# Performance work log

Measured on AMD Instinct MI355X. Metric: run time of the kernel, lower is better.

Reference implementation:

```python
import jax, jax.numpy as jnp
import numpy as np

N_NODES = 100000
N_FEAT = 512
HIDDEN = 16
N_CLASSES = 7
N_EDGES = 3200000


def gcn_conv(x, W, b, src, dst, num_nodes):
    """GCNConv: add self-loops, symmetric deg^-1/2 normalization, linear, aggregate."""
    loop = jnp.arange(num_nodes, dtype=src.dtype)
    src2 = jnp.concatenate([src, loop])  # [E+N]
    dst2 = jnp.concatenate([dst, loop])
    ones = jnp.ones(src2.shape[0], dtype=x.dtype)
    deg = jax.ops.segment_sum(ones, dst2, num_segments=num_nodes)  # in-degree incl. self-loop
    dinv = jnp.where(deg > 0, jax.lax.rsqrt(deg), 0.0)
    norm = dinv[src2] * dinv[dst2]  # [E+N]
    h = x @ W  # [N, out] -- transform before gather (small out dim)
    msg = h[src2] * norm[:, None]  # gather + scale
    out = jax.ops.segment_sum(msg, dst2, num_segments=num_nodes)  # scatter-add
    return out + b


def setup_inputs() -> dict:
    key = jax.random.key(0)
    k1, k2, k3, k4, k5 = jax.random.split(key, 5)
    x = jax.random.normal(k1, (N_NODES, N_FEAT), dtype=jnp.float32)
    edge_index = jax.random.randint(k2, (2, N_EDGES), 0, N_NODES, dtype=jnp.int64)
    # Glorot init like PyG GCNConv
    W1 = jax.random.normal(k3, (N_FEAT, HIDDEN), dtype=jnp.float32) * np.sqrt(2.0 / (N_FEAT + HIDDEN))
    b1 = jnp.zeros((HIDDEN,), dtype=jnp.float32)
    W2 = jax.random.normal(k4, (HIDDEN, N_CLASSES), dtype=jnp.float32) * np.sqrt(2.0 / (HIDDEN + N_CLASSES))
    b2 = jnp.zeros((N_CLASSES,), dtype=jnp.float32)
    return {"x": x, "edge_index": edge_index, "W1": W1, "b1": b1, "W2": W2, "b2": b2}


def reference(x, edge_index, W1, b1, W2, b2):
    src, dst = edge_index[0], edge_index[1]
    h = gcn_conv(x, W1, b1, src, dst, N_NODES)
    h = jax.nn.relu(h)
    # F.dropout(training=self.training): identity in eval mode (deterministic reference)
    h = gcn_conv(h, W2, b2, src, dst, N_NODES)
    return jax.nn.log_softmax(h, axis=1)
```

## Files before the change

kernel.cpp:

```cpp
#include <hip/hip_runtime.h>
#include <math.h>

#define N_NODES   100000
#define N_FEAT    512
#define HIDDEN    16
#define N_CLASSES 7
#define N_EDGES   3200000

#define BSHIFT 7
#define BNODES 128
#define BMASK  127
#define NBUK   782
#define CHUNK  16384
#define NCHUNK 196
#define CAP    6144

typedef short v8s __attribute__((ext_vector_type(8)));
typedef float v4f __attribute__((ext_vector_type(4)));

__device__ __forceinline__ float bf_lo(unsigned int p) { return __uint_as_float(p << 16); }
__device__ __forceinline__ float bf_hi(unsigned int p) { return __uint_as_float(p & 0xffff0000u); }
__device__ __forceinline__ unsigned int pack_bf2(float a, float b) {
    unsigned int ua = __float_as_uint(a); ua += 0x7fffu + ((ua >> 16) & 1u);
    unsigned int ub = __float_as_uint(b); ub += 0x7fffu + ((ub >> 16) & 1u);
    return (ua >> 16) | (ub & 0xffff0000u);
}


__global__ __launch_bounds__(1024) void k_hist(const int* __restrict__ dst,
                                               int* __restrict__ hglob) {
    __shared__ int h[NBUK];
    int tid = threadIdx.x;
    for (int i = tid; i < NBUK; i += 1024) h[i] = 0;
    __syncthreads();
    int base = blockIdx.x * CHUNK;
    for (int i = tid; i < CHUNK; i += 1024) {
        int e = base + i;
        if (e < N_EDGES) atomicAdd(&h[dst[e] >> BSHIFT], 1);
    }
    __syncthreads();
    for (int i = tid; i < NBUK; i += 1024)
        hglob[blockIdx.x * NBUK + i] = h[i];
}


__global__ __launch_bounds__(1024) void k_scan(const int* __restrict__ hglob,
                                               int* __restrict__ btot,
                                               int* __restrict__ gbase,
                                               int* __restrict__ hpre) {
    __shared__ int sd[1024];
    int t = threadIdx.x;
    int tot = 0;
    if (t < NBUK)
        for (int c = 0; c < NCHUNK; c++) tot += hglob[c * NBUK + t];
    sd[t] = (t < NBUK) ? tot : 0;
    __syncthreads();
    for (int off = 1; off < 1024; off <<= 1) {
        int a = (t >= off) ? sd[t - off] : 0;
        __syncthreads();
        sd[t] += a;
        __syncthreads();
    }
    if (t < NBUK) {
        int ex = sd[t] - tot;
        btot[t] = tot;
        gbase[t] = ex;
        int run = ex;
        for (int c = 0; c < NCHUNK; c++) {
            hpre[c * NBUK + t] = run;
            run += hglob[c * NBUK + t];
        }
    }
}


__global__ __launch_bounds__(1024) void k_scatter(const int* __restrict__ src,
                                                  const int* __restrict__ dst,
                                                  const int* __restrict__ hpre,
                                                  int* __restrict__ entries) {
    __shared__ int lb[NBUK];
    __shared__ int cur[NBUK];
    int tid = threadIdx.x;
    for (int i = tid; i < NBUK; i += 1024) {
        lb[i] = hpre[blockIdx.x * NBUK + i];
        cur[i] = 0;
    }
    __syncthreads();
    int base = blockIdx.x * CHUNK;
    for (int i = tid; i < CHUNK; i += 1024) {
        int e = base + i;
        if (e < N_EDGES) {
            int d = dst[e];
            int b = d >> BSHIFT;
            int pos = lb[b] + atomicAdd(&cur[b], 1);
            entries[pos] = src[e] | ((d & BMASK) << 17);
        }
    }
}


__global__ __launch_bounds__(512) void k_nodesort(int* __restrict__ entries,
                                                  const int* __restrict__ btot,
                                                  const int* __restrict__ gbase,
                                                  float* __restrict__ dinv,
                                                  int* __restrict__ nodeptr) {
    __shared__ int ebuf[CAP];
    __shared__ int hcnt[BNODES];
    __shared__ int hincl[BNODES];
    __shared__ int hcur[BNODES];
    int tid = threadIdx.x;
    int bk = blockIdx.x;
    int cnt = btot[bk], base = gbase[bk];
    if (cnt > CAP) cnt = CAP;
    if (tid < BNODES) hcnt[tid] = 0;
    __syncthreads();
    for (int i = tid; i < cnt; i += 512) {
        int en = entries[base + i];
        ebuf[i] = en;
        atomicAdd(&hcnt[en >> 17], 1);
    }
    __syncthreads();
    if (tid < BNODES) hincl[tid] = hcnt[tid];
    __syncthreads();
    for (int off = 1; off < BNODES; off <<= 1) {
        int v = 0;
        if (tid < BNODES && tid >= off) v = hincl[tid - off];
        __syncthreads();
        if (tid < BNODES) hincl[tid] += v;
        __syncthreads();
    }
    if (tid < BNODES) {
        int excl = hincl[tid] - hcnt[tid];
        hcur[tid] = excl;
        int n = bk * BNODES + tid;
        if (n < N_NODES) {
            nodeptr[n] = base + excl;
            dinv[n]    = rsqrtf((float)(hcnt[tid] + 1));
        } else if (n == N_NODES) {
            nodeptr[n] = base + excl;
        }
    }
    __syncthreads();
    for (int i = tid; i < cnt; i += 512) {
        int en = ebuf[i];
        int pos = atomicAdd(&hcur[en >> 17], 1);
        entries[base + pos] = en & 0x1FFFF;
    }
}


__global__ __launch_bounds__(256) void k_gemm1(const float* __restrict__ x,
                                               const float* __restrict__ W1,
                                               const float* __restrict__ dinv,
                                               unsigned int* __restrict__ hs1b) {
    __shared__ unsigned int wfrag[16 * 64 * 4];
    __shared__ unsigned int atile[64 * 68];

    int tid = threadIdx.x;
    int wave = tid >> 6, lane = tid & 63;
    int row0 = blockIdx.x * 64;
    int m = lane & 15, quad = lane >> 4;

    {
        int q0 = tid * 4;
#pragma unroll
        for (int qq = 0; qq < 4; qq++) {
            int q = q0 + qq;
            int s = q >> 6, l = q & 63;
            int n = l & 15, kb = s * 32 + (l >> 4) * 8;
            unsigned int* wp = &wfrag[q * 4];
#pragma unroll
            for (int h = 0; h < 4; h++)
                wp[h] = pack_bf2(W1[(kb + 2 * h) * 16 + n],
                                 W1[(kb + 2 * h + 1) * 16 + n]);
        }
    }

    v4f acc = {0.f, 0.f, 0.f, 0.f};

    for (int c = 0; c < 4; c++) {
        __syncthreads();
#pragma unroll
        for (int i = 0; i < 8; i++) {
            int f = i * 256 + tid;
            int r = f >> 5, c4 = f & 31;
            int grow = row0 + r;
            float4 xv = make_float4(0.f, 0.f, 0.f, 0.f);
            if (grow < N_NODES)
                xv = *(const float4*)(x + (size_t)grow * N_FEAT + c * 128 + c4 * 4);
            unsigned int* ap = &atile[r * 68 + c4 * 2];
            ap[0] = pack_bf2(xv.x, xv.y);
            ap[1] = pack_bf2(xv.z, xv.w);
        }
        __syncthreads();
#pragma unroll
        for (int s = 0; s < 4; s++) {
            v8s af = *(const v8s*)&atile[(wave * 16 + m) * 68 + s * 16 + quad * 4];
            v8s bf = *(const v8s*)&wfrag[((c * 4 + s) * 64 + lane) * 4];
            acc = __builtin_amdgcn_mfma_f32_16x16x32_bf16(af, bf, acc, 0, 0, 0);
        }
    }

    __syncthreads();
    float* dt = (float*)atile;
    {
        float* wdt = dt + wave * 272;
        int col = lane & 15;
#pragma unroll
        for (int r = 0; r < 4; r++)
            wdt[(quad * 4 + r) * 17 + col] = acc[r];
    }
    __syncthreads();
    {
        int row = tid >> 2, p = tid & 3;
        int grow = row0 + row;
        if (grow < N_NODES) {
            float dn = dinv[grow];
            float* wdt = dt + (row >> 4) * 272 + (row & 15) * 17 + 4 * p;
            unsigned int d0 = pack_bf2(dn * wdt[0], dn * wdt[1]);
            unsigned int d1 = pack_bf2(dn * wdt[2], dn * wdt[3]);
            *(uint2*)(hs1b + (size_t)grow * 8 + 2 * p) = make_uint2(d0, d1);
        }
    }
}


__global__ __launch_bounds__(512) void k_agg1(const unsigned int* __restrict__ hs1b,
                                              const int* __restrict__ srt,
                                              const int* __restrict__ nodeptr,
                                              const float* __restrict__ dinv,
                                              const float* __restrict__ b1,
                                              const float* __restrict__ W2,
                                              unsigned int* __restrict__ hs2b) {
    __shared__ float w2l[HIDDEN * N_CLASSES];
    __shared__ float b1l[HIDDEN];
    __shared__ float part[BNODES][17];
    int tid = threadIdx.x;
    if (tid < HIDDEN * N_CLASSES) w2l[tid] = W2[tid];
    if (tid < HIDDEN) b1l[tid] = b1[tid];

    int bk = blockIdx.x;
    int g = tid >> 1, j = tid & 1;
    int l = g & (BNODES - 1), half = g >> 7;
    int n = bk * BNODES + l;
    bool valid = (n < N_NODES);

    float accL[4] = {0.f, 0.f, 0.f, 0.f};
    float accH[4] = {0.f, 0.f, 0.f, 0.f};
    const uint4* hv = (const uint4*)hs1b;

    if (valid) {
        int p0 = nodeptr[n], p1 = nodeptr[n + 1];
        int mid = p0 + ((p1 - p0) >> 1);
        int e0 = half ? mid : p0;
        int e1 = half ? p1 : mid;
        int e = e0;
        for (; e + 4 <= e1; e += 4) {
            int s[4];
            uint4 v[4];
#pragma unroll
            for (int u = 0; u < 4; u++) s[u] = srt[e + u];
#pragma unroll
            for (int u = 0; u < 4; u++) v[u] = hv[(size_t)s[u] * 2 + j];
#pragma unroll
            for (int u = 0; u < 4; u++) {
                accL[0] += bf_lo(v[u].x); accH[0] += bf_hi(v[u].x);
                accL[1] += bf_lo(v[u].y); accH[1] += bf_hi(v[u].y);
                accL[2] += bf_lo(v[u].z); accH[2] += bf_hi(v[u].z);
                accL[3] += bf_lo(v[u].w); accH[3] += bf_hi(v[u].w);
            }
        }
        for (; e < e1; e++) {
            uint4 v0 = hv[(size_t)srt[e] * 2 + j];
            accL[0] += bf_lo(v0.x); accH[0] += bf_hi(v0.x);
            accL[1] += bf_lo(v0.y); accH[1] += bf_hi(v0.y);
            accL[2] += bf_lo(v0.z); accH[2] += bf_hi(v0.z);
            accL[3] += bf_lo(v0.w); accH[3] += bf_hi(v0.w);
        }
        if (half == 0) {
            uint4 sv = hv[(size_t)n * 2 + j];
            accL[0] += bf_lo(sv.x); accH[0] += bf_hi(sv.x);
            accL[1] += bf_lo(sv.y); accH[1] += bf_hi(sv.y);
            accL[2] += bf_lo(sv.z); accH[2] += bf_hi(sv.z);
            accL[3] += bf_lo(sv.w); accH[3] += bf_hi(sv.w);
        }
    }

    if (half == 1 && valid) {
#pragma unroll
        for (int q = 0; q < 4; q++) {
            int ch = j * 8 + 2 * q;
            part[l][ch]     = accL[q];
            part[l][ch + 1] = accH[q];
        }
    }
    __syncthreads();

    if (half == 0 && valid) {
        float dn = dinv[n];
        float t[7] = {0.f, 0.f, 0.f, 0.f, 0.f, 0.f, 0.f};
#pragma unroll
        for (int q = 0; q < 4; q++) {
            int ch = j * 8 + 2 * q;
            float z0 = fmaxf(dn * (accL[q] + part[l][ch])     + b1l[ch],     0.f);
            float z1 = fmaxf(dn * (accH[q] + part[l][ch + 1]) + b1l[ch + 1], 0.f);
            const float* w0 = &w2l[ch * 7];
            const float* w1 = &w2l[(ch + 1) * 7];
#pragma unroll
            for (int k = 0; k < 7; k++) t[k] += z0 * w0[k] + z1 * w1[k];
        }
#pragma unroll
        for (int k = 0; k < 7; k++) t[k] += __shfl_xor(t[k], 1, 64);
        if (j == 0) {
            uint4 o;
            o.x = pack_bf2(dn * t[0], dn * t[1]);
            o.y = pack_bf2(dn * t[2], dn * t[3]);
            o.z = pack_bf2(dn * t[4], dn * t[5]);
            o.w = pack_bf2(dn * t[6], 0.f);
            ((uint4*)hs2b)[n] = o;
        }
    }
}


__global__ __launch_bounds__(512) void k_agg2(const unsigned int* __restrict__ hs2b,
                                              const int* __restrict__ srt,
                                              const int* __restrict__ nodeptr,
                                              const float* __restrict__ dinv,
                                              const float* __restrict__ b2,
                                              float* __restrict__ out) {
    int tid = threadIdx.x;
    int bk = blockIdx.x;
    int l = tid >> 2, h = tid & 3;
    int n = bk * BNODES + l;
    bool valid = (n < N_NODES);

    float a[8] = {0.f, 0.f, 0.f, 0.f, 0.f, 0.f, 0.f, 0.f};
    const uint4* hv = (const uint4*)hs2b;

    if (valid) {
        int p0 = nodeptr[n], p1 = nodeptr[n + 1];
        int deg = p1 - p0;
        int e0 = p0 + ((deg * h) >> 2);
        int e1 = p0 + ((deg * (h + 1)) >> 2);
        int e = e0;
        for (; e + 4 <= e1; e += 4) {
            int s[4];
            uint4 v[4];
#pragma unroll
            for (int u = 0; u < 4; u++) s[u] = srt[e + u];
#pragma unroll
            for (int u = 0; u < 4; u++) v[u] = hv[s[u]];
#pragma unroll
            for (int u = 0; u < 4; u++) {
                a[0] += bf_lo(v[u].x); a[1] += bf_hi(v[u].x);
                a[2] += bf_lo(v[u].y); a[3] += bf_hi(v[u].y);
                a[4] += bf_lo(v[u].z); a[5] += bf_hi(v[u].z);
                a[6] += bf_lo(v[u].w);
            }
        }
        for (; e < e1; e++) {
            uint4 v0 = hv[srt[e]];
            a[0] += bf_lo(v0.x); a[1] += bf_hi(v0.x);
            a[2] += bf_lo(v0.y); a[3] += bf_hi(v0.y);
            a[4] += bf_lo(v0.z); a[5] += bf_hi(v0.z);
            a[6] += bf_lo(v0.w);
        }
        if (h == 0) {
            uint4 sv = hv[n];
            a[0] += bf_lo(sv.x); a[1] += bf_hi(sv.x);
            a[2] += bf_lo(sv.y); a[3] += bf_hi(sv.y);
            a[4] += bf_lo(sv.z); a[5] += bf_hi(sv.z);
            a[6] += bf_lo(sv.w);
        }
#pragma unroll
        for (int q = 0; q < 7; q++) {
            a[q] += __shfl_xor(a[q], 1, 64);
            a[q] += __shfl_xor(a[q], 2, 64);
        }
        if (h == 0) {
            float dn = dinv[n];
            float lg[7];
#pragma unroll
            for (int c = 0; c < 7; c++) lg[c] = dn * a[c] + b2[c];
            float m = lg[0];
#pragma unroll
            for (int c = 1; c < 7; c++) m = fmaxf(m, lg[c]);
            float s = 0.f;
#pragma unroll
            for (int c = 0; c < 7; c++) s += expf(lg[c] - m);
            float ls = m + logf(s);
#pragma unroll
            for (int c = 0; c < 7; c++) out[(size_t)n * 7 + c] = lg[c] - ls;
        }
    }
}


extern "C" void kernel_launch(void* const* d_in, const int* in_sizes, int n_in,
                              void* d_out, int out_size, void* d_ws, size_t ws_size,
                              hipStream_t stream) {
    const float* x  = (const float*)d_in[0];
    const int*   ei = (const int*)d_in[1];
    const float* W1 = (const float*)d_in[2];
    const float* b1 = (const float*)d_in[3];
    const float* W2 = (const float*)d_in[4];
    const float* b2 = (const float*)d_in[5];
    float* out = (float*)d_out;

    const int* src = ei;
    const int* dst = ei + N_EDGES;

    char* w = (char*)d_ws;
    int*          btot    = (int*)(w + 0);
    int*          gbase   = (int*)(w + 4096);
    float*        dinv    = (float*)(w + 8192);
    int*          nodeptr = (int*)(w + 408576);
    int*          hglob   = (int*)(w + 808960);
    int*          hpre    = (int*)(w + 1422336);
    unsigned int* hs1b    = (unsigned int*)(w + 2036736);
    unsigned int* hs2b    = (unsigned int*)(w + 5236736);
    int*          entries = (int*)(w + 6836736);

    k_hist    <<<NCHUNK, 1024, 0, stream>>>(dst, hglob);
    k_scan    <<<1, 1024, 0, stream>>>(hglob, btot, gbase, hpre);
    k_scatter <<<NCHUNK, 1024, 0, stream>>>(src, dst, hpre, entries);
    k_nodesort<<<NBUK, 512, 0, stream>>>(entries, btot, gbase, dinv, nodeptr);
    k_gemm1   <<<1563, 256, 0, stream>>>(x, W1, dinv, hs1b);
    k_agg1    <<<NBUK, 512, 0, stream>>>(hs1b, entries, nodeptr, dinv, b1, W2, hs2b);
    k_agg2    <<<NBUK, 512, 0, stream>>>(hs2b, entries, nodeptr, dinv, b2, out);
}
```

Before: 456.9 us.

## Drop per-node sort; aggregate bucket edges via shared-memory atomics

```diff
diff --git a/kernel.cpp b/kernel.cpp
--- a/kernel.cpp
+++ b/kernel.cpp
@@ -13,7 +13,6 @@
 #define NBUK   782
 #define CHUNK  16384
 #define NCHUNK 196
-#define CAP    6144
 
 typedef short v8s __attribute__((ext_vector_type(8)));
 typedef float v4f __attribute__((ext_vector_type(4)));
@@ -99,52 +98,22 @@
 }
 
 
-__global__ __launch_bounds__(512) void k_nodesort(int* __restrict__ entries,
-                                                  const int* __restrict__ btot,
-                                                  const int* __restrict__ gbase,
-                                                  float* __restrict__ dinv,
-                                                  int* __restrict__ nodeptr) {
-    __shared__ int ebuf[CAP];
+__global__ __launch_bounds__(256) void k_deg(const int* __restrict__ entries,
+                                             const int* __restrict__ btot,
+                                             const int* __restrict__ gbase,
+                                             float* __restrict__ dinv) {
     __shared__ int hcnt[BNODES];
-    __shared__ int hincl[BNODES];
-    __shared__ int hcur[BNODES];
     int tid = threadIdx.x;
     int bk = blockIdx.x;
+    if (tid < BNODES) hcnt[tid] = 0;
+    __syncthreads();
     int cnt = btot[bk], base = gbase[bk];
-    if (cnt > CAP) cnt = CAP;
-    if (tid < BNODES) hcnt[tid] = 0;
-    __syncthreads();
-    for (int i = tid; i < cnt; i += 512) {
-        int en = entries[base + i];
-        ebuf[i] = en;
-        atomicAdd(&hcnt[en >> 17], 1);
-    }
-    __syncthreads();
-    if (tid < BNODES) hincl[tid] = hcnt[tid];
-    __syncthreads();
-    for (int off = 1; off < BNODES; off <<= 1) {
-        int v = 0;
-        if (tid < BNODES && tid >= off) v = hincl[tid - off];
-        __syncthreads();
-        if (tid < BNODES) hincl[tid] += v;
-        __syncthreads();
-    }
+    for (int i = tid; i < cnt; i += 256)
+        atomicAdd(&hcnt[entries[base + i] >> 17], 1);
+    __syncthreads();
     if (tid < BNODES) {
-        int excl = hincl[tid] - hcnt[tid];
-        hcur[tid] = excl;
         int n = bk * BNODES + tid;
-        if (n < N_NODES) {
-            nodeptr[n] = base + excl;
-            dinv[n]    = rsqrtf((float)(hcnt[tid] + 1));
-        } else if (n == N_NODES) {
-            nodeptr[n] = base + excl;
-        }
-    }
-    __syncthreads();
-    for (int i = tid; i < cnt; i += 512) {
-        int en = ebuf[i];
-        int pos = atomicAdd(&hcur[en >> 17], 1);
-        entries[base + pos] = en & 0x1FFFF;
+        if (n < N_NODES) dinv[n] = rsqrtf((float)(hcnt[tid] + 1));
     }
 }
 
@@ -225,164 +194,139 @@
 }
 
 
+__device__ __forceinline__ void acc16(float* A, uint4 va, uint4 vb) {
+    atomicAdd(&A[0],  bf_lo(va.x)); atomicAdd(&A[1],  bf_hi(va.x));
+    atomicAdd(&A[2],  bf_lo(va.y)); atomicAdd(&A[3],  bf_hi(va.y));
+    atomicAdd(&A[4],  bf_lo(va.z)); atomicAdd(&A[5],  bf_hi(va.z));
+    atomicAdd(&A[6],  bf_lo(va.w)); atomicAdd(&A[7],  bf_hi(va.w));
+    atomicAdd(&A[8],  bf_lo(vb.x)); atomicAdd(&A[9],  bf_hi(vb.x));
+    atomicAdd(&A[10], bf_lo(vb.y)); atomicAdd(&A[11], bf_hi(vb.y));
+    atomicAdd(&A[12], bf_lo(vb.z)); atomicAdd(&A[13], bf_hi(vb.z));
+    atomicAdd(&A[14], bf_lo(vb.w)); atomicAdd(&A[15], bf_hi(vb.w));
+}
+
 __global__ __launch_bounds__(512) void k_agg1(const unsigned int* __restrict__ hs1b,
-                                              const int* __restrict__ srt,
-                                              const int* __restrict__ nodeptr,
+                                              const int* __restrict__ entries,
+                                              const int* __restrict__ btot,
+                                              const int* __restrict__ gbase,
                                               const float* __restrict__ dinv,
                                               const float* __restrict__ b1,
                                               const float* __restrict__ W2,
                                               unsigned int* __restrict__ hs2b) {
+    __shared__ float acc[BNODES][17];
     __shared__ float w2l[HIDDEN * N_CLASSES];
     __shared__ float b1l[HIDDEN];
-    __shared__ float part[BNODES][17];
-    int tid = threadIdx.x;
+    int tid = threadIdx.x;
+    int bk = blockIdx.x;
     if (tid < HIDDEN * N_CLASSES) w2l[tid] = W2[tid];
     if (tid < HIDDEN) b1l[tid] = b1[tid];
-
-    int bk = blockIdx.x;
-    int g = tid >> 1, j = tid & 1;
-    int l = g & (BNODES - 1), half = g >> 7;
-    int n = bk * BNODES + l;
-    bool valid = (n < N_NODES);
-
-    float accL[4] = {0.f, 0.f, 0.f, 0.f};
-    float accH[4] = {0.f, 0.f, 0.f, 0.f};
+    for (int i = tid; i < BNODES * 17; i += 512) ((float*)acc)[i] = 0.f;
+    __syncthreads();
+
+    int cnt = btot[bk], base = gbase[bk];
     const uint4* hv = (const uint4*)hs1b;
 
-    if (valid) {
-        int p0 = nodeptr[n], p1 = nodeptr[n + 1];
-        int mid = p0 + ((p1 - p0) >> 1);
-        int e0 = half ? mid : p0;
-        int e1 = half ? p1 : mid;
-        int e = e0;
-        for (; e + 4 <= e1; e += 4) {
-            int s[4];
-            uint4 v[4];
-#pragma unroll
-            for (int u = 0; u < 4; u++) s[u] = srt[e + u];
-#pragma unroll
-            for (int u = 0; u < 4; u++) v[u] = hv[(size_t)s[u] * 2 + j];
-#pragma unroll
-            for (int u = 0; u < 4; u++) {
-                accL[0] += bf_lo(v[u].x); accH[0] += bf_hi(v[u].x);
-                accL[1] += bf_lo(v[u].y); accH[1] += bf_hi(v[u].y);
-                accL[2] += bf_lo(v[u].z); accH[2] += bf_hi(v[u].z);
-                accL[3] += bf_lo(v[u].w); accH[3] += bf_hi(v[u].w);
+    int i = tid;
+    for (; i + 512 < cnt; i += 1024) {
+        int e0 = entries[base + i];
+        int e1 = entries[base + i + 512];
+        int s0 = e0 & 0x1FFFF, s1 = e1 & 0x1FFFF;
+        uint4 va0 = hv[(size_t)s0 * 2],     va1 = hv[(size_t)s1 * 2];
+        uint4 vb0 = hv[(size_t)s0 * 2 + 1], vb1 = hv[(size_t)s1 * 2 + 1];
+        acc16(acc[e0 >> 17], va0, vb0);
+        acc16(acc[e1 >> 17], va1, vb1);
+    }
+    if (i < cnt) {
+        int e0 = entries[base + i];
+        int s0 = e0 & 0x1FFFF;
+        uint4 va0 = hv[(size_t)s0 * 2];
+        uint4 vb0 = hv[(size_t)s0 * 2 + 1];
+        acc16(acc[e0 >> 17], va0, vb0);
+    }
+    __syncthreads();
+
+    if (tid < 2 * BNODES) {
+        int l = tid >> 1, j = tid & 1;
+        int n = bk * BNODES + l;
+        if (n < N_NODES) {
+            float dn = dinv[n];
+            uint4 sv = hv[(size_t)n * 2 + j];
+            float se[8] = {bf_lo(sv.x), bf_hi(sv.x), bf_lo(sv.y), bf_hi(sv.y),
+                           bf_lo(sv.z), bf_hi(sv.z), bf_lo(sv.w), bf_hi(sv.w)};
+            float t[7] = {0.f, 0.f, 0.f, 0.f, 0.f, 0.f, 0.f};
+#pragma unroll
+            for (int q = 0; q < 8; q++) {
+                int ch = j * 8 + q;
+                float z = fmaxf(dn * (acc[l][ch] + se[q]) + b1l[ch], 0.f);
+                const float* wr = &w2l[ch * 7];
+#pragma unroll
+                for (int k = 0; k < 7; k++) t[k] += z * wr[k];
             }
-        }
-        for (; e < e1; e++) {
-            uint4 v0 = hv[(size_t)srt[e] * 2 + j];
-            accL[0] += bf_lo(v0.x); accH[0] += bf_hi(v0.x);
-            accL[1] += bf_lo(v0.y); accH[1] += bf_hi(v0.y);
-            accL[2] += bf_lo(v0.z); accH[2] += bf_hi(v0.z);
-            accL[3] += bf_lo(v0.w); accH[3] += bf_hi(v0.w);
-        }
-        if (half == 0) {
-            uint4 sv = hv[(size_t)n * 2 + j];
-            accL[0] += bf_lo(sv.x); accH[0] += bf_hi(sv.x);
-            accL[1] += bf_lo(sv.y); accH[1] += bf_hi(sv.y);
-            accL[2] += bf_lo(sv.z); accH[2] += bf_hi(sv.z);
-            accL[3] += bf_lo(sv.w); accH[3] += bf_hi(sv.w);
-        }
-    }
-
-    if (half == 1 && valid) {
-#pragma unroll
-        for (int q = 0; q < 4; q++) {
-            int ch = j * 8 + 2 * q;
-            part[l][ch]     = accL[q];
-            part[l][ch + 1] = accH[q];
-        }
-    }
-    __syncthreads();
-
-    if (half == 0 && valid) {
-        float dn = dinv[n];
-        float t[7] = {0.f, 0.f, 0.f, 0.f, 0.f, 0.f, 0.f};
-#pragma unroll
-        for (int q = 0; q < 4; q++) {
-            int ch = j * 8 + 2 * q;
-            float z0 = fmaxf(dn * (accL[q] + part[l][ch])     + b1l[ch],     0.f);
-            float z1 = fmaxf(dn * (accH[q] + part[l][ch + 1]) + b1l[ch + 1], 0.f);
-            const float* w0 = &w2l[ch * 7];
-            const float* w1 = &w2l[(ch + 1) * 7];
-#pragma unroll
-            for (int k = 0; k < 7; k++) t[k] += z0 * w0[k] + z1 * w1[k];
-        }
-#pragma unroll
-        for (int k = 0; k < 7; k++) t[k] += __shfl_xor(t[k], 1, 64);
-        if (j == 0) {
-            uint4 o;
-            o.x = pack_bf2(dn * t[0], dn * t[1]);
-            o.y = pack_bf2(dn * t[2], dn * t[3]);
-            o.z = pack_bf2(dn * t[4], dn * t[5]);
-            o.w = pack_bf2(dn * t[6], 0.f);
-            ((uint4*)hs2b)[n] = o;
-        }
-    }
-}
-
+#pragma unroll
+            for (int k = 0; k < 7; k++) t[k] += __shfl_xor(t[k], 1, 64);
+            if (j == 0) {
+                uint4 o;
+                o.x = pack_bf2(dn * t[0], dn * t[1]);
+                o.y = pack_bf2(dn * t[2], dn * t[3]);
+                o.z = pack_bf2(dn * t[4], dn * t[5]);
+                o.w = pack_bf2(dn * t[6], 0.f);
+                ((uint4*)hs2b)[n] = o;
+            }
+        }
+    }
+}
+
+
+__device__ __forceinline__ void acc7(float* A, uint4 v) {
+    atomicAdd(&A[0], bf_lo(v.x)); atomicAdd(&A[1], bf_hi(v.x));
+    atomicAdd(&A[2], bf_lo(v.y)); atomicAdd(&A[3], bf_hi(v.y));
+    atomicAdd(&A[4], bf_lo(v.z)); atomicAdd(&A[5], bf_hi(v.z));
+    atomicAdd(&A[6], bf_lo(v.w));
+}
 
 __global__ __launch_bounds__(512) void k_agg2(const unsigned int* __restrict__ hs2b,
-                                              const int* __restrict__ srt,
-                                              const int* __restrict__ nodeptr,
+                                              const int* __restrict__ entries,
+                                              const int* __restrict__ btot,
+                                              const int* __restrict__ gbase,
                                               const float* __restrict__ dinv,
                                               const float* __restrict__ b2,
                                               float* __restrict__ out) {
+    __shared__ float acc[BNODES][9];
+    __shared__ float so[BNODES * 7];
     int tid = threadIdx.x;
     int bk = blockIdx.x;
-    int l = tid >> 2, h = tid & 3;
-    int n = bk * BNODES + l;
-    bool valid = (n < N_NODES);
-
-    float a[8] = {0.f, 0.f, 0.f, 0.f, 0.f, 0.f, 0.f, 0.f};
+    for (int i = tid; i < BNODES * 9; i += 512) ((float*)acc)[i] = 0.f;
+    __syncthreads();
+
+    int cnt = btot[bk], base = gbase[bk];
     const uint4* hv = (const uint4*)hs2b;
 
-    if (valid) {
-        int p0 = nodeptr[n], p1 = nodeptr[n + 1];
-        int deg = p1 - p0;
-        int e0 = p0 + ((deg * h) >> 2);
-        int e1 = p0 + ((deg * (h + 1)) >> 2);
-        int e = e0;
-        for (; e + 4 <= e1; e += 4) {
-            int s[4];
-            uint4 v[4];
-#pragma unroll
-            for (int u = 0; u < 4; u++) s[u] = srt[e + u];
-#pragma unroll
-            for (int u = 0; u < 4; u++) v[u] = hv[s[u]];
-#pragma unroll
-            for (int u = 0; u < 4; u++) {
-                a[0] += bf_lo(v[u].x); a[1] += bf_hi(v[u].x);
-                a[2] += bf_lo(v[u].y); a[3] += bf_hi(v[u].y);
-                a[4] += bf_lo(v[u].z); a[5] += bf_hi(v[u].z);
-                a[6] += bf_lo(v[u].w);
-            }
-        }
-        for (; e < e1; e++) {
-            uint4 v0 = hv[srt[e]];
-            a[0] += bf_lo(v0.x); a[1] += bf_hi(v0.x);
-            a[2] += bf_lo(v0.y); a[3] += bf_hi(v0.y);
-            a[4] += bf_lo(v0.z); a[5] += bf_hi(v0.z);
-            a[6] += bf_lo(v0.w);
-        }
-        if (h == 0) {
+    int i = tid;
+    for (; i + 512 < cnt; i += 1024) {
+        int e0 = entries[base + i];
+        int e1 = entries[base + i + 512];
+        uint4 v0 = hv[e0 & 0x1FFFF];
+        uint4 v1 = hv[e1 & 0x1FFFF];
+        acc7(acc[e0 >> 17], v0);
+        acc7(acc[e1 >> 17], v1);
+    }
+    if (i < cnt) {
+        int e0 = entries[base + i];
+        uint4 v0 = hv[e0 & 0x1FFFF];
+        acc7(acc[e0 >> 17], v0);
+    }
+    __syncthreads();
+
+    if (tid < BNODES) {
+        int n = bk * BNODES + tid;
+        if (n < N_NODES) {
+            float dn = dinv[n];
             uint4 sv = hv[n];
-            a[0] += bf_lo(sv.x); a[1] += bf_hi(sv.x);
-            a[2] += bf_lo(sv.y); a[3] += bf_hi(sv.y);
-            a[4] += bf_lo(sv.z); a[5] += bf_hi(sv.z);
-            a[6] += bf_lo(sv.w);
-        }
-#pragma unroll
-        for (int q = 0; q < 7; q++) {
-            a[q] += __shfl_xor(a[q], 1, 64);
-            a[q] += __shfl_xor(a[q], 2, 64);
-        }
-        if (h == 0) {
-            float dn = dinv[n];
+            float se[7] = {bf_lo(sv.x), bf_hi(sv.x), bf_lo(sv.y), bf_hi(sv.y),
+                           bf_lo(sv.z), bf_hi(sv.z), bf_lo(sv.w)};
             float lg[7];
 #pragma unroll
-            for (int c = 0; c < 7; c++) lg[c] = dn * a[c] + b2[c];
+            for (int c = 0; c < 7; c++) lg[c] = dn * (acc[tid][c] + se[c]) + b2[c];
             float m = lg[0];
 #pragma unroll
             for (int c = 1; c < 7; c++) m = fmaxf(m, lg[c]);
@@ -391,9 +335,16 @@
             for (int c = 0; c < 7; c++) s += expf(lg[c] - m);
             float ls = m + logf(s);
 #pragma unroll
-            for (int c = 0; c < 7; c++) out[(size_t)n * 7 + c] = lg[c] - ls;
-        }
-    }
+            for (int c = 0; c < 7; c++) so[tid * 7 + c] = lg[c] - ls;
+        }
+    }
+    __syncthreads();
+
+    int nvalid = N_NODES - bk * BNODES;
+    if (nvalid > BNODES) nvalid = BNODES;
+    int vout = nvalid * 7;
+    for (int idx = tid; idx < vout; idx += 512)
+        out[(size_t)bk * (BNODES * 7) + idx] = so[idx];
 }
 
 
@@ -415,7 +366,6 @@
     int*          btot    = (int*)(w + 0);
     int*          gbase   = (int*)(w + 4096);
     float*        dinv    = (float*)(w + 8192);
-    int*          nodeptr = (int*)(w + 408576);
     int*          hglob   = (int*)(w + 808960);
     int*          hpre    = (int*)(w + 1422336);
     unsigned int* hs1b    = (unsigned int*)(w + 2036736);
@@ -425,8 +375,8 @@
     k_hist    <<<NCHUNK, 1024, 0, stream>>>(dst, hglob);
     k_scan    <<<1, 1024, 0, stream>>>(hglob, btot, gbase, hpre);
     k_scatter <<<NCHUNK, 1024, 0, stream>>>(src, dst, hpre, entries);
-    k_nodesort<<<NBUK, 512, 0, stream>>>(entries, btot, gbase, dinv, nodeptr);
+    k_deg     <<<NBUK, 256, 0, stream>>>(entries, btot, gbase, dinv);
     k_gemm1   <<<1563, 256, 0, stream>>>(x, W1, dinv, hs1b);
-    k_agg1    <<<NBUK, 512, 0, stream>>>(hs1b, entries, nodeptr, dinv, b1, W2, hs2b);
-    k_agg2    <<<NBUK, 512, 0, stream>>>(hs2b, entries, nodeptr, dinv, b2, out);
-}
+    k_agg1    <<<NBUK, 512, 0, stream>>>(hs1b, entries, btot, gbase, dinv, b1, W2, hs2b);
+    k_agg2    <<<NBUK, 512, 0, stream>>>(hs2b, entries, btot, gbase, dinv, b2, out);
+}
```

Measured after the change: 878.8 us. 92.3% more time.

## Stage scatter entries in shared memory by bucket before global write

Applied to the files above, without the earlier changes.

```diff
diff --git a/kernel.cpp b/kernel.cpp
--- a/kernel.cpp
+++ b/kernel.cpp
@@ -80,21 +80,66 @@
                                                   int* __restrict__ entries) {
     __shared__ int lb[NBUK];
     __shared__ int cur[NBUK];
-    int tid = threadIdx.x;
+    __shared__ int lbase[NBUK];
+    __shared__ int sd[1024];
+    __shared__ int sbuf[CHUNK];
+    __shared__ unsigned short sbk[CHUNK];
+    int tid = threadIdx.x;
+    int base = blockIdx.x * CHUNK;
+
     for (int i = tid; i < NBUK; i += 1024) {
         lb[i] = hpre[blockIdx.x * NBUK + i];
         cur[i] = 0;
     }
     __syncthreads();
-    int base = blockIdx.x * CHUNK;
-    for (int i = tid; i < CHUNK; i += 1024) {
-        int e = base + i;
+
+    int myent[16];
+    int mypos[16];
+#pragma unroll
+    for (int u = 0; u < 16; u++) {
+        int e = base + u * 1024 + tid;
+        int en = 0, bp = -1;
         if (e < N_EDGES) {
             int d = dst[e];
             int b = d >> BSHIFT;
-            int pos = lb[b] + atomicAdd(&cur[b], 1);
-            entries[pos] = src[e] | ((d & BMASK) << 17);
-        }
+            int r = atomicAdd(&cur[b], 1);
+            en = src[e] | ((d & BMASK) << 17);
+            bp = (b << 14) | r;
+        }
+        myent[u] = en;
+        mypos[u] = bp;
+    }
+    __syncthreads();
+
+    int v = (tid < NBUK) ? cur[tid] : 0;
+    sd[tid] = v;
+    __syncthreads();
+    for (int off = 1; off < 1024; off <<= 1) {
+        int a = (tid >= off) ? sd[tid - off] : 0;
+        __syncthreads();
+        sd[tid] += a;
+        __syncthreads();
+    }
+    if (tid < NBUK) lbase[tid] = sd[tid] - v;
+    __syncthreads();
+
+#pragma unroll
+    for (int u = 0; u < 16; u++) {
+        int bp = mypos[u];
+        if (bp >= 0) {
+            int b = bp >> 14, r = bp & 0x3FFF;
+            int p = lbase[b] + r;
+            sbuf[p] = myent[u];
+            sbk[p] = (unsigned short)b;
+        }
+    }
+    __syncthreads();
+
+    int lim = N_EDGES - base;
+    if (lim > CHUNK) lim = CHUNK;
+    for (int i = tid; i < lim; i += 1024) {
+        int b = sbk[i];
+        entries[lb[b] + (i - lbase[b])] = sbuf[i];
     }
 }
 
```

Measured after the change: 435.2 us. 1.05x faster.
